# Optimization experiments

Hardware: AMD Instinct MI355X
Metric: run time of the kernel (lower is better)

The kernel has to match this reference:

```python
import jax, jax.numpy as jnp
import numpy as np

B, L, S, H, E, D = 2, 2048, 2048, 16, 64, 64


def setup_inputs() -> dict:
    key = jax.random.key(0)
    kq, kk, kv = jax.random.split(key, 3)
    queries = jax.random.normal(kq, (B, L, H, E), dtype=jnp.float32)
    keys = jax.random.normal(kk, (B, S, H, E), dtype=jnp.float32)
    values = jax.random.normal(kv, (B, S, H, D), dtype=jnp.float32)
    # causal mask: True = masked out (matches masked_fill semantics)
    causal = jnp.triu(jnp.ones((L, S), dtype=bool), k=1)
    attn_mask = jnp.broadcast_to(causal, (B, L, S))
    return {"queries": queries, "keys": keys, "values": values, "attn_mask": attn_mask}


def reference(queries, keys, values, attn_mask):
    # queries: [B,L,H,E], keys: [B,S,H,E], values: [B,S,H,D], attn_mask: [B,L,S] bool
    E_ = queries.shape[-1]
    scale = 1.0 / jnp.sqrt(jnp.asarray(E_, dtype=queries.dtype))
    scores = jnp.einsum('blhe,bshe->bhls', queries, keys)  # [B,H,L,S]
    scores = jnp.where(attn_mask[:, None, :, :], -jnp.inf, scores)
    A = jax.nn.softmax(scale * scores, axis=-1)
    A = jnp.nan_to_num(A)  # fully-masked rows -> 0 (dropout prob is 0.0)
    V = jnp.einsum('bhls,bshd->blhd', A, values)  # [B,L,H,D]
    return (V, A)
```

## Files before the change

kernel.cpp:

```cpp
#include <hip/hip_runtime.h>
#include <cstdint>
#include <cstddef>

#define B_ 2
#define L_ 2048
#define S_ 2048
#define H_ 16
#define E_ 64
#define D_ 64

#define LOG2E_SCALE 0.18033688011112042f

typedef __attribute__((ext_vector_type(8))) short short8;
typedef __attribute__((ext_vector_type(4))) float float4v;
typedef __attribute__((ext_vector_type(4))) unsigned short ushort4v;

__device__ __forceinline__ unsigned short f2bf(float f) {
  unsigned u = __builtin_bit_cast(unsigned, f);
  u += 0x7FFFu + ((u >> 16) & 1u);
  return (unsigned short)(u >> 16);
}

__device__ __forceinline__ float myexp2(float x) {
#if __has_builtin(__builtin_amdgcn_exp2f)
  return __builtin_amdgcn_exp2f(x);
#else
  return exp2f(x);
#endif
}

__global__ __launch_bounds__(256)
void conv_nh_kernel(const float* __restrict__ in, unsigned short* __restrict__ out) {
  unsigned idx4 = blockIdx.x * 256u + threadIdx.x;
  unsigned e4 = idx4 & 15u;
  unsigned h  = (idx4 >> 4) & 15u;
  unsigned n  = (idx4 >> 8) & 2047u;
  unsigned b  = idx4 >> 19;
  float4v v = *(const float4v*)(in + (size_t)idx4 * 4u);
  ushort4v o;
  o.x = f2bf(v.x); o.y = f2bf(v.y); o.z = f2bf(v.z); o.w = f2bf(v.w);
  *(ushort4v*)(out + (((size_t)(b * H_ + h) * 2048u + n) * 16u + e4) * 4u) = o;
}

__global__ __launch_bounds__(256)
void conv_vt_kernel(const float* __restrict__ V, unsigned short* __restrict__ VT) {
  __shared__ float tile[64 * 65];
  const int st = blockIdx.x, h = blockIdx.y, b = blockIdx.z;
  const int tid = threadIdx.x;
  const float* vb = V + ((size_t)(b * S_ + st * 64) * H_ + h) * D_;
  #pragma unroll
  for (int i = 0; i < 4; ++i) {
    int e = tid + i * 256;
    int row = e >> 4, c4 = (e & 15) * 4;
    float4v v = *(const float4v*)(vb + (size_t)row * (H_ * D_) + c4);
    tile[row * 65 + c4 + 0] = v.x; tile[row * 65 + c4 + 1] = v.y;
    tile[row * 65 + c4 + 2] = v.z; tile[row * 65 + c4 + 3] = v.w;
  }
  __syncthreads();
  #pragma unroll
  for (int i = 0; i < 4; ++i) {
    int e = tid + i * 256;
    int d = e >> 4, c4 = (e & 15) * 4;
    ushort4v o;
    o.x = f2bf(tile[(c4 + 0) * 65 + d]); o.y = f2bf(tile[(c4 + 1) * 65 + d]);
    o.z = f2bf(tile[(c4 + 2) * 65 + d]); o.w = f2bf(tile[(c4 + 3) * 65 + d]);
    *(ushort4v*)(VT + ((size_t)(b * H_ + h) * D_ + d) * S_ + st * 64 + c4) = o;
  }
}

__global__ __launch_bounds__(256, 6)
void fullattn4_kernel(const unsigned short* __restrict__ Qbf,
                      const unsigned short* __restrict__ Kbf,
                      const unsigned short* __restrict__ VT,
                      float* __restrict__ OutV, float* __restrict__ OutA) {
  __shared__ alignas(16) char smem[18688];
  unsigned short* Ps = (unsigned short*)smem;
  float* Lbuf = (float*)(smem + 18432);
  float* Obuf = (float*)smem;

  const int tid = threadIdx.x;
  const int w = tid >> 6;
  const int lane = tid & 63;
  const int quad = lane >> 4;
  const int n16 = lane & 15;

  const int st = (int)(gridDim.x - 1u - blockIdx.x);
  const int h = blockIdx.y, b = blockIdx.z;
  const int l0 = st * 16;
  const int jt = st >> 2;
  const int doff = (st & 3) * 16;

  float* arow0 = OutA + ((size_t)((b * H_ + h) * L_) + l0) * (size_t)S_;

  {
    const int c4start = (jt + 1) * 16;
    #pragma unroll
    for (int i = 0; i < 4; ++i) {
      float4v* rp = (float4v*)(arow0 + (size_t)(w * 4 + i) * S_);
      for (int c4 = c4start + lane; c4 < S_ / 4; c4 += 64) {
        float4v z = {0.f, 0.f, 0.f, 0.f};
        __builtin_nontemporal_store(z, rp + c4);
      }
    }
  }

  const unsigned short* qrow = Qbf + ((size_t)(b * H_ + h) * L_ + l0 + n16) * E_;
  const short8 aQ0 = *(const short8*)(qrow + quad * 8);
  const short8 aQ1 = *(const short8*)(qrow + 32 + quad * 8);

  const unsigned short* kbase = Kbf + (size_t)(b * H_ + h) * S_ * E_;
  const unsigned short* vbase = VT + (size_t)(b * H_ + h) * D_ * S_;

  float lsum[4] = {0.f, 0.f, 0.f, 0.f};
  for (int j = w; j <= jt; j += 4) {
    const unsigned short* kb = kbase + (size_t)j * 64 * E_;
    #pragma unroll
    for (int t = 0; t < 4; ++t) {
      const unsigned short* kr = kb + (size_t)(t * 16 + n16) * E_;
      const short8 b0 = *(const short8*)(kr + quad * 8);
      const short8 b1 = *(const short8*)(kr + 32 + quad * 8);
      float4v acc = {0.f, 0.f, 0.f, 0.f};
      acc = __builtin_amdgcn_mfma_f32_16x16x32_bf16(aQ0, b0, acc, 0, 0, 0);
      acc = __builtin_amdgcn_mfma_f32_16x16x32_bf16(aQ1, b1, acc, 0, 0, 0);
      #pragma unroll
      for (int r = 0; r < 4; ++r) {
        float x = acc[r] * LOG2E_SCALE;
        if (j == jt && (t * 16 + n16 > doff + quad * 4 + r)) x = -__builtin_inff();
        lsum[r] += myexp2(x);
      }
    }
  }
  #pragma unroll
  for (int off = 1; off <= 8; off <<= 1)
    #pragma unroll
    for (int r = 0; r < 4; ++r) lsum[r] += __shfl_xor(lsum[r], off);
  if (n16 == 0) {
    #pragma unroll
    for (int r = 0; r < 4; ++r) Lbuf[w * 16 + quad * 4 + r] = lsum[r];
  }
  __syncthreads();
  float inv_l[4];
  #pragma unroll
  for (int r = 0; r < 4; ++r) {
    const int row = quad * 4 + r;
    inv_l[r] = 1.0f / (Lbuf[row] + Lbuf[16 + row] + Lbuf[32 + row] + Lbuf[48 + row]);
  }

  float4v oacc[4];
  #pragma unroll
  for (int t2 = 0; t2 < 4; ++t2) oacc[t2] = (float4v){0.f, 0.f, 0.f, 0.f};

  int par = 0;
  for (int j = w; j <= jt; j += 4, par ^= 1) {
    const unsigned short* kb = kbase + (size_t)j * 64 * E_;
    unsigned short* psw = Ps + (size_t)((w << 1) | par) * (16 * 72);
    float* arow = arow0 + (size_t)(quad * 4) * S_ + j * 64 + n16;
    #pragma unroll
    for (int t = 0; t < 4; ++t) {
      const unsigned short* kr = kb + (size_t)(t * 16 + n16) * E_;
      const short8 b0 = *(const short8*)(kr + quad * 8);
      const short8 b1 = *(const short8*)(kr + 32 + quad * 8);
      float4v acc = {0.f, 0.f, 0.f, 0.f};
      acc = __builtin_amdgcn_mfma_f32_16x16x32_bf16(aQ0, b0, acc, 0, 0, 0);
      acc = __builtin_amdgcn_mfma_f32_16x16x32_bf16(aQ1, b1, acc, 0, 0, 0);
      #pragma unroll
      for (int r = 0; r < 4; ++r) {
        float p = myexp2(acc[r] * LOG2E_SCALE) * inv_l[r];
        if (j == jt && (t * 16 + n16 > doff + quad * 4 + r)) p = 0.f;
        __builtin_nontemporal_store(p, arow + (size_t)r * S_ + t * 16);
        float pp = __shfl_xor(p, 1);
        unsigned short sp = f2bf(p), spp = f2bf(pp);
        unsigned dw = (n16 & 1) ? ((unsigned)spp | ((unsigned)sp << 16))
                                : ((unsigned)sp | ((unsigned)spp << 16));
        *(unsigned*)&psw[(quad * 4 + r) * 72 + (t * 16 + (n16 & ~1))] = dw;
      }
    }
    __builtin_amdgcn_wave_barrier();
    const short8 aP0 = *(const short8*)&psw[n16 * 72 + quad * 8];
    const short8 aP1 = *(const short8*)&psw[n16 * 72 + 32 + quad * 8];
    #pragma unroll
    for (int t2 = 0; t2 < 4; ++t2) {
      const unsigned short* vr = vbase + (size_t)(t2 * 16 + n16) * S_ + j * 64;
      const short8 v0 = *(const short8*)(vr + quad * 8);
      const short8 v1 = *(const short8*)(vr + 32 + quad * 8);
      oacc[t2] = __builtin_amdgcn_mfma_f32_16x16x32_bf16(aP0, v0, oacc[t2], 0, 0, 0);
      oacc[t2] = __builtin_amdgcn_mfma_f32_16x16x32_bf16(aP1, v1, oacc[t2], 0, 0, 0);
    }
  }

  __syncthreads();
  #pragma unroll
  for (int t2 = 0; t2 < 4; ++t2)
    #pragma unroll
    for (int r = 0; r < 4; ++r)
      Obuf[(size_t)(w * 16 + quad * 4 + r) * 68 + t2 * 16 + n16] = oacc[t2][r];
  __syncthreads();
  {
    const int row = tid >> 4;
    const int c0 = (tid & 15) * 4;
    float4v s = *(const float4v*)&Obuf[(size_t)row * 68 + c0];
    #pragma unroll
    for (int ww = 1; ww < 4; ++ww) {
      float4v t = *(const float4v*)&Obuf[(size_t)(ww * 16 + row) * 68 + c0];
      s.x += t.x; s.y += t.y; s.z += t.z; s.w += t.w;
    }
    float* op = OutV + ((size_t)(b * L_ + l0 + row) * H_ + h) * D_ + c0;
    __builtin_nontemporal_store(s, (float4v*)op);
  }
}

__global__ __launch_bounds__(256, 4)
void fullattn_fb_kernel(const float* __restrict__ Q, const float* __restrict__ K,
                        const float* __restrict__ V, float* __restrict__ OutV,
                        float* __restrict__ OutA) {
  __shared__ alignas(16) unsigned short Qs[64 * 72];
  __shared__ alignas(16) unsigned short Ks[64 * 72];
  __shared__ alignas(16) unsigned short VTs[64 * 72];
  __shared__ alignas(16) unsigned short Ps[64 * 72];
  const int tid = threadIdx.x;
  const int w = tid >> 6, lane = tid & 63, quad = lane >> 4, n16 = lane & 15;
  const int lt = (int)(gridDim.x - 1u - blockIdx.x);
  const int h = blockIdx.y, b = blockIdx.z;
  const int l0 = lt * 64;
  float* arow0 = OutA + ((size_t)((b * H_ + h) * L_) + l0) * (size_t)S_;
  {
    const int c4start = (lt + 1) * 16;
    for (int rr = w; rr < 64; rr += 4) {
      float4v* rp = (float4v*)(arow0 + (size_t)rr * S_);
      for (int c4 = c4start + lane; c4 < S_ / 4; c4 += 64) {
        float4v z = {0.f, 0.f, 0.f, 0.f};
        __builtin_nontemporal_store(z, rp + c4);
      }
    }
  }
  {
    const float* qb = Q + ((size_t)(b * L_ + l0) * H_ + h) * E_;
    #pragma unroll
    for (int i = 0; i < 4; ++i) {
      int e = tid + i * 256;
      int row = e >> 4, c4 = (e & 15) * 4;
      float4v qv = *(const float4v*)(qb + (size_t)row * (H_ * E_) + c4);
      ushort4v o; o.x = f2bf(qv.x); o.y = f2bf(qv.y); o.z = f2bf(qv.z); o.w = f2bf(qv.w);
      *(ushort4v*)&Qs[row * 72 + c4] = o;
    }
  }
  auto stageK = [&](int j) {
    const float* kb = K + ((size_t)(b * S_ + j * 64) * H_ + h) * E_;
    #pragma unroll
    for (int i = 0; i < 4; ++i) {
      int e = tid + i * 256;
      int row = e >> 4, c4 = (e & 15) * 4;
      float4v kv = *(const float4v*)(kb + (size_t)row * (H_ * E_) + c4);
      ushort4v o; o.x = f2bf(kv.x); o.y = f2bf(kv.y); o.z = f2bf(kv.z); o.w = f2bf(kv.w);
      *(ushort4v*)&Ks[row * 72 + c4] = o;
    }
  };
  auto stageV = [&](int j) {
    const float* vb = V + ((size_t)(b * S_ + j * 64) * H_ + h) * D_;
    const int d = lane;
    #pragma unroll
    for (int i = 0; i < 8; ++i) {
      int s2 = w * 8 + i;
      float f0 = vb[(size_t)(2 * s2) * (H_ * D_) + d];
      float f1 = vb[(size_t)(2 * s2 + 1) * (H_ * D_) + d];
      unsigned pk = (unsigned)f2bf(f0) | ((unsigned)f2bf(f1) << 16);
      *(unsigned*)&VTs[d * 72 + 2 * s2] = pk;
    }
  };
  __syncthreads();
  const short8 aQ0 = *(const short8*)&Qs[(w * 16 + n16) * 72 + quad * 8];
  const short8 aQ1 = *(const short8*)&Qs[(w * 16 + n16) * 72 + 32 + quad * 8];
  float m2[4], lsum[4];
  #pragma unroll
  for (int r = 0; r < 4; ++r) { m2[r] = -__builtin_inff(); lsum[r] = 0.f; }
  for (int j = 0; j <= lt; ++j) {
    stageK(j);
    __syncthreads();
    float x[4][4];
    #pragma unroll
    for (int t = 0; t < 4; ++t) {
      const short8 b0 = *(const short8*)&Ks[(t * 16 + n16) * 72 + quad * 8];
      const short8 b1 = *(const short8*)&Ks[(t * 16 + n16) * 72 + 32 + quad * 8];
      float4v acc = {0.f, 0.f, 0.f, 0.f};
      acc = __builtin_amdgcn_mfma_f32_16x16x32_bf16(aQ0, b0, acc, 0, 0, 0);
      acc = __builtin_amdgcn_mfma_f32_16x16x32_bf16(aQ1, b1, acc, 0, 0, 0);
      #pragma unroll
      for (int r = 0; r < 4; ++r) x[t][r] = acc[r] * LOG2E_SCALE;
    }
    if (j == lt) {
      #pragma unroll
      for (int t = 0; t < 4; ++t)
        #pragma unroll
        for (int r = 0; r < 4; ++r)
          if (t * 16 + n16 > w * 16 + quad * 4 + r) x[t][r] = -__builtin_inff();
    }
    #pragma unroll
    for (int r = 0; r < 4; ++r) {
      float mx = fmaxf(fmaxf(x[0][r], x[1][r]), fmaxf(x[2][r], x[3][r]));
      #pragma unroll
      for (int off = 8; off >= 1; off >>= 1) mx = fmaxf(mx, __shfl_xor(mx, off));
      float mnew = fmaxf(m2[r], mx);
      float alpha = myexp2(m2[r] - mnew);
      float sm = myexp2(x[0][r] - mnew) + myexp2(x[1][r] - mnew) +
                 myexp2(x[2][r] - mnew) + myexp2(x[3][r] - mnew);
      #pragma unroll
      for (int off = 8; off >= 1; off >>= 1) sm += __shfl_xor(sm, off);
      lsum[r] = lsum[r] * alpha + sm;
      m2[r] = mnew;
    }
    __syncthreads();
  }
  float inv_l[4];
  #pragma unroll
  for (int r = 0; r < 4; ++r) inv_l[r] = 1.0f / lsum[r];
  float4v oacc[4];
  #pragma unroll
  for (int t2 = 0; t2 < 4; ++t2) oacc[t2] = (float4v){0.f, 0.f, 0.f, 0.f};
  for (int j = 0; j <= lt; ++j) {
    stageK(j);
    stageV(j);
    __syncthreads();
    float* arow = arow0 + (size_t)(w * 16 + quad * 4) * S_ + j * 64 + n16;
    #pragma unroll
    for (int t = 0; t < 4; ++t) {
      const short8 b0 = *(const short8*)&Ks[(t * 16 + n16) * 72 + quad * 8];
      const short8 b1 = *(const short8*)&Ks[(t * 16 + n16) * 72 + 32 + quad * 8];
      float4v acc = {0.f, 0.f, 0.f, 0.f};
      acc = __builtin_amdgcn_mfma_f32_16x16x32_bf16(aQ0, b0, acc, 0, 0, 0);
      acc = __builtin_amdgcn_mfma_f32_16x16x32_bf16(aQ1, b1, acc, 0, 0, 0);
      #pragma unroll
      for (int r = 0; r < 4; ++r) {
        float p = myexp2(acc[r] * LOG2E_SCALE - m2[r]) * inv_l[r];
        if (j == lt && (t * 16 + n16 > w * 16 + quad * 4 + r)) p = 0.f;
        __builtin_nontemporal_store(p, arow + (size_t)r * S_ + t * 16);
        float pp = __shfl_xor(p, 1);
        unsigned short sp = f2bf(p), spp = f2bf(pp);
        unsigned dw = (n16 & 1) ? ((unsigned)spp | ((unsigned)sp << 16))
                                : ((unsigned)sp | ((unsigned)spp << 16));
        *(unsigned*)&Ps[(w * 16 + quad * 4 + r) * 72 + (t * 16 + (n16 & ~1))] = dw;
      }
    }
    __builtin_amdgcn_wave_barrier();
    const short8 aP0 = *(const short8*)&Ps[(w * 16 + n16) * 72 + quad * 8];
    const short8 aP1 = *(const short8*)&Ps[(w * 16 + n16) * 72 + 32 + quad * 8];
    #pragma unroll
    for (int t2 = 0; t2 < 4; ++t2) {
      const short8 v0 = *(const short8*)&VTs[(t2 * 16 + n16) * 72 + quad * 8];
      const short8 v1 = *(const short8*)&VTs[(t2 * 16 + n16) * 72 + 32 + quad * 8];
      oacc[t2] = __builtin_amdgcn_mfma_f32_16x16x32_bf16(aP0, v0, oacc[t2], 0, 0, 0);
      oacc[t2] = __builtin_amdgcn_mfma_f32_16x16x32_bf16(aP1, v1, oacc[t2], 0, 0, 0);
    }
    __syncthreads();
  }
  float* ob = OutV + ((size_t)(b * L_ + l0 + w * 16 + quad * 4) * H_ + h) * D_ + n16;
  #pragma unroll
  for (int t2 = 0; t2 < 4; ++t2)
    #pragma unroll
    for (int r = 0; r < 4; ++r)
      __builtin_nontemporal_store(oacc[t2][r], ob + (size_t)r * (H_ * D_) + t2 * 16);
}

extern "C" void kernel_launch(void* const* d_in, const int* in_sizes, int n_in,
                              void* d_out, int out_size, void* d_ws, size_t ws_size,
                              hipStream_t stream) {
  (void)in_sizes; (void)n_in; (void)out_size;
  const float* Q = (const float*)d_in[0];
  const float* K = (const float*)d_in[1];
  const float* V = (const float*)d_in[2];
  float* OutV = (float*)d_out;
  float* OutA = (float*)d_out + (size_t)B_ * L_ * H_ * D_;

  const size_t bytes_each = (size_t)B_ * H_ * 2048 * 64 * sizeof(unsigned short);
  if (ws_size >= 3 * bytes_each) {
    unsigned short* Qbf = (unsigned short*)d_ws;
    unsigned short* Kbf = (unsigned short*)((char*)d_ws + bytes_each);
    unsigned short* VTb = (unsigned short*)((char*)d_ws + 2 * bytes_each);
    const int nblk = (B_ * 2048 * H_ * E_ / 4) / 256;
    conv_nh_kernel<<<nblk, 256, 0, stream>>>(Q, Qbf);
    conv_nh_kernel<<<nblk, 256, 0, stream>>>(K, Kbf);
    conv_vt_kernel<<<dim3(S_ / 64, H_, B_), 256, 0, stream>>>(V, VTb);
    fullattn4_kernel<<<dim3(L_ / 16, H_, B_), 256, 0, stream>>>(Qbf, Kbf, VTb, OutV, OutA);
  } else {
    fullattn_fb_kernel<<<dim3(L_ / 64, H_, B_), 256, 0, stream>>>(Q, K, V, OutV, OutA);
  }
}
```

Before: 755.3 us.

## Transpose QK MFMA operands for row-contiguous P, prefetch K and V tiles

Swaps the MFMA operand order so each lane holds four consecutive key columns of one query row. The probability matrix can then be written as float4 nontemporal stores, and the bf16 P tile is packed into LDS without cross-lane shuffles. The row-sum pass now double-buffers K tile loads in registers, and the PV pass issues V loads before the QK compute. Launch bounds drop to four blocks per SM to make room for the extra prefetch registers, which may reduce occupancy.

```diff
diff --git a/kernel.cpp b/kernel.cpp
--- a/kernel.cpp
+++ b/kernel.cpp
@@ -14,6 +14,7 @@
 typedef __attribute__((ext_vector_type(8))) short short8;
 typedef __attribute__((ext_vector_type(4))) float float4v;
 typedef __attribute__((ext_vector_type(4))) unsigned short ushort4v;
+typedef __attribute__((ext_vector_type(2))) unsigned int uint2v;
 
 __device__ __forceinline__ unsigned short f2bf(float f) {
   unsigned u = __builtin_bit_cast(unsigned, f);
@@ -68,8 +69,8 @@
   }
 }
 
-__global__ __launch_bounds__(256, 6)
-void fullattn4_kernel(const unsigned short* __restrict__ Qbf,
+__global__ __launch_bounds__(256, 4)
+void fullattn5_kernel(const unsigned short* __restrict__ Qbf,
                       const unsigned short* __restrict__ Kbf,
                       const unsigned short* __restrict__ VT,
                       float* __restrict__ OutV, float* __restrict__ OutA) {
@@ -105,86 +106,107 @@
   }
 
   const unsigned short* qrow = Qbf + ((size_t)(b * H_ + h) * L_ + l0 + n16) * E_;
-  const short8 aQ0 = *(const short8*)(qrow + quad * 8);
-  const short8 aQ1 = *(const short8*)(qrow + 32 + quad * 8);
+  const short8 qB0 = *(const short8*)(qrow + quad * 8);
+  const short8 qB1 = *(const short8*)(qrow + 32 + quad * 8);
 
   const unsigned short* kbase = Kbf + (size_t)(b * H_ + h) * S_ * E_;
   const unsigned short* vbase = VT + (size_t)(b * H_ + h) * D_ * S_;
 
-  float lsum[4] = {0.f, 0.f, 0.f, 0.f};
-  for (int j = w; j <= jt; j += 4) {
+  float lsum = 0.f;
+
+  short8 kA0[4], kA1[4], kB0[4], kB1[4];
+  auto loadK = [&](int j, short8 (&b0)[4], short8 (&b1)[4]) {
     const unsigned short* kb = kbase + (size_t)j * 64 * E_;
+    #pragma unroll
+    for (int t = 0; t < 4; ++t) {
+      const unsigned short* kr = kb + (size_t)(t * 16 + n16) * E_;
+      b0[t] = *(const short8*)(kr + quad * 8);
+      b1[t] = *(const short8*)(kr + 32 + quad * 8);
+    }
+  };
+
+  auto procK = [&](const short8 (&b0)[4], const short8 (&b1)[4], int j) {
+    #pragma unroll
+    for (int t = 0; t < 4; ++t) {
+      float4v acc = {0.f, 0.f, 0.f, 0.f};
+      acc = __builtin_amdgcn_mfma_f32_16x16x32_bf16(b0[t], qB0, acc, 0, 0, 0);
+      acc = __builtin_amdgcn_mfma_f32_16x16x32_bf16(b1[t], qB1, acc, 0, 0, 0);
+      #pragma unroll
+      for (int r = 0; r < 4; ++r) {
+        float x = acc[r] * LOG2E_SCALE;
+        if (j == jt && (t * 16 + quad * 4 + r > doff + n16)) x = -__builtin_inff();
+        lsum += myexp2(x);
+      }
+    }
+  };
+
+  if (w <= jt) {
+    loadK(w, kA0, kA1);
+    int j = w;
+    for (;;) {
+      if (j + 4 <= jt) loadK(j + 4, kB0, kB1);
+      procK(kA0, kA1, j);
+      j += 4;
+      if (j > jt) break;
+      if (j + 4 <= jt) loadK(j + 4, kA0, kA1);
+      procK(kB0, kB1, j);
+      j += 4;
+      if (j > jt) break;
+    }
+  }
+
+  lsum += __shfl_xor(lsum, 16);
+  lsum += __shfl_xor(lsum, 32);
+  if (quad == 0) Lbuf[w * 16 + n16] = lsum;
+  __syncthreads();
+  const float inv_l = 1.0f / (Lbuf[n16] + Lbuf[16 + n16] + Lbuf[32 + n16] + Lbuf[48 + n16]);
+
+  float4v oacc[4];
+  #pragma unroll
+  for (int t2 = 0; t2 < 4; ++t2) oacc[t2] = (float4v){0.f, 0.f, 0.f, 0.f};
+
+  float* arowL = arow0 + (size_t)n16 * S_ + quad * 4;
+
+  int par = 0;
+  for (int j = w; j <= jt; j += 4, par ^= 1) {
+    short8 v0f[4], v1f[4];
+    #pragma unroll
+    for (int t2 = 0; t2 < 4; ++t2) {
+      const unsigned short* vr = vbase + (size_t)(t2 * 16 + n16) * S_ + j * 64;
+      v0f[t2] = *(const short8*)(vr + quad * 8);
+      v1f[t2] = *(const short8*)(vr + 32 + quad * 8);
+    }
+
+    const unsigned short* kb = kbase + (size_t)j * 64 * E_;
+    unsigned short* psw = Ps + (size_t)((w << 1) | par) * (16 * 72);
     #pragma unroll
     for (int t = 0; t < 4; ++t) {
       const unsigned short* kr = kb + (size_t)(t * 16 + n16) * E_;
       const short8 b0 = *(const short8*)(kr + quad * 8);
       const short8 b1 = *(const short8*)(kr + 32 + quad * 8);
       float4v acc = {0.f, 0.f, 0.f, 0.f};
-      acc = __builtin_amdgcn_mfma_f32_16x16x32_bf16(aQ0, b0, acc, 0, 0, 0);
-      acc = __builtin_amdgcn_mfma_f32_16x16x32_bf16(aQ1, b1, acc, 0, 0, 0);
+      acc = __builtin_amdgcn_mfma_f32_16x16x32_bf16(b0, qB0, acc, 0, 0, 0);
+      acc = __builtin_amdgcn_mfma_f32_16x16x32_bf16(b1, qB1, acc, 0, 0, 0);
+      float p[4];
       #pragma unroll
       for (int r = 0; r < 4; ++r) {
-        float x = acc[r] * LOG2E_SCALE;
-        if (j == jt && (t * 16 + n16 > doff + quad * 4 + r)) x = -__builtin_inff();
-        lsum[r] += myexp2(x);
+        p[r] = myexp2(acc[r] * LOG2E_SCALE) * inv_l;
+        if (j == jt && (t * 16 + quad * 4 + r > doff + n16)) p[r] = 0.f;
       }
-    }
-  }
-  #pragma unroll
-  for (int off = 1; off <= 8; off <<= 1)
-    #pragma unroll
-    for (int r = 0; r < 4; ++r) lsum[r] += __shfl_xor(lsum[r], off);
-  if (n16 == 0) {
-    #pragma unroll
-    for (int r = 0; r < 4; ++r) Lbuf[w * 16 + quad * 4 + r] = lsum[r];
-  }
-  __syncthreads();
-  float inv_l[4];
-  #pragma unroll
-  for (int r = 0; r < 4; ++r) {
-    const int row = quad * 4 + r;
-    inv_l[r] = 1.0f / (Lbuf[row] + Lbuf[16 + row] + Lbuf[32 + row] + Lbuf[48 + row]);
-  }
-
-  float4v oacc[4];
-  #pragma unroll
-  for (int t2 = 0; t2 < 4; ++t2) oacc[t2] = (float4v){0.f, 0.f, 0.f, 0.f};
-
-  int par = 0;
-  for (int j = w; j <= jt; j += 4, par ^= 1) {
-    const unsigned short* kb = kbase + (size_t)j * 64 * E_;
-    unsigned short* psw = Ps + (size_t)((w << 1) | par) * (16 * 72);
-    float* arow = arow0 + (size_t)(quad * 4) * S_ + j * 64 + n16;
-    #pragma unroll
-    for (int t = 0; t < 4; ++t) {
-      const unsigned short* kr = kb + (size_t)(t * 16 + n16) * E_;
-      const short8 b0 = *(const short8*)(kr + quad * 8);
-      const short8 b1 = *(const short8*)(kr + 32 + quad * 8);
-      float4v acc = {0.f, 0.f, 0.f, 0.f};
-      acc = __builtin_amdgcn_mfma_f32_16x16x32_bf16(aQ0, b0, acc, 0, 0, 0);
-      acc = __builtin_amdgcn_mfma_f32_16x16x32_bf16(aQ1, b1, acc, 0, 0, 0);
-      #pragma unroll
-      for (int r = 0; r < 4; ++r) {
-        float p = myexp2(acc[r] * LOG2E_SCALE) * inv_l[r];
-        if (j == jt && (t * 16 + n16 > doff + quad * 4 + r)) p = 0.f;
-        __builtin_nontemporal_store(p, arow + (size_t)r * S_ + t * 16);
-        float pp = __shfl_xor(p, 1);
-        unsigned short sp = f2bf(p), spp = f2bf(pp);
-        unsigned dw = (n16 & 1) ? ((unsigned)spp | ((unsigned)sp << 16))
-                                : ((unsigned)sp | ((unsigned)spp << 16));
-        *(unsigned*)&psw[(quad * 4 + r) * 72 + (t * 16 + (n16 & ~1))] = dw;
-      }
+      float4v p4 = {p[0], p[1], p[2], p[3]};
+      __builtin_nontemporal_store(p4, (float4v*)(arowL + j * 64 + t * 16));
+      uint2v dw;
+      dw.x = (unsigned)f2bf(p[0]) | ((unsigned)f2bf(p[1]) << 16);
+      dw.y = (unsigned)f2bf(p[2]) | ((unsigned)f2bf(p[3]) << 16);
+      *(uint2v*)&psw[n16 * 72 + t * 16 + quad * 4] = dw;
     }
     __builtin_amdgcn_wave_barrier();
     const short8 aP0 = *(const short8*)&psw[n16 * 72 + quad * 8];
     const short8 aP1 = *(const short8*)&psw[n16 * 72 + 32 + quad * 8];
     #pragma unroll
     for (int t2 = 0; t2 < 4; ++t2) {
-      const unsigned short* vr = vbase + (size_t)(t2 * 16 + n16) * S_ + j * 64;
-      const short8 v0 = *(const short8*)(vr + quad * 8);
-      const short8 v1 = *(const short8*)(vr + 32 + quad * 8);
-      oacc[t2] = __builtin_amdgcn_mfma_f32_16x16x32_bf16(aP0, v0, oacc[t2], 0, 0, 0);
-      oacc[t2] = __builtin_amdgcn_mfma_f32_16x16x32_bf16(aP1, v1, oacc[t2], 0, 0, 0);
+      oacc[t2] = __builtin_amdgcn_mfma_f32_16x16x32_bf16(aP0, v0f[t2], oacc[t2], 0, 0, 0);
+      oacc[t2] = __builtin_amdgcn_mfma_f32_16x16x32_bf16(aP1, v1f[t2], oacc[t2], 0, 0, 0);
     }
   }
 
@@ -379,7 +401,7 @@
     conv_nh_kernel<<<nblk, 256, 0, stream>>>(Q, Qbf);
     conv_nh_kernel<<<nblk, 256, 0, stream>>>(K, Kbf);
     conv_vt_kernel<<<dim3(S_ / 64, H_, B_), 256, 0, stream>>>(V, VTb);
-    fullattn4_kernel<<<dim3(L_ / 16, H_, B_), 256, 0, stream>>>(Qbf, Kbf, VTb, OutV, OutA);
+    fullattn5_kernel<<<dim3(L_ / 16, H_, B_), 256, 0, stream>>>(Qbf, Kbf, VTb, OutV, OutA);
   } else {
     fullattn_fb_kernel<<<dim3(L_ / 64, H_, B_), 256, 0, stream>>>(Q, K, V, OutV, OutA);
   }
```

New measurement: 745.5 us. No clear change (-1.3%).
